# Kernel tuning notes

Measured on AMD Instinct MI355X. Metric: run time of the kernel, lower is better.

The kernel has to match this reference:

```python
import jax, jax.numpy as jnp
import numpy as np
from jax import lax

NUM_LAYERS = 128
SEQ_LEN = 256
H = 1  # hidden_size = input_size = 1


def setup_inputs() -> dict:
    key = jax.random.key(0)
    k = jax.random.split(key, 5)
    # PyTorch GRU init: U(-1/sqrt(H), 1/sqrt(H)) with H=1 -> U(-1, 1)
    u = lambda kk, shp: jax.random.uniform(kk, shp, jnp.float32, -1.0, 1.0)
    return {
        "x": jax.random.normal(k[0], (1, SEQ_LEN), jnp.float32),
        "w_ih": u(k[1], (NUM_LAYERS, 3 * H, H)),  # gates stacked [r, z, n]
        "w_hh": u(k[2], (NUM_LAYERS, 3 * H, H)),
        "b_ih": u(k[3], (NUM_LAYERS, 3 * H)),
        "b_hh": u(k[4], (NUM_LAYERS, 3 * H)),
    }


def _gru_stack(x_seq, w_ih, w_hh, b_ih, b_hh):
    # x_seq: [T, H]; params stacked over layers. PyTorch GRU equations, gate order r,z,n.
    def layer_step(seq, params):
        wi, wh, bi, bh = params  # [3H,H], [3H,H], [3H], [3H]

        def cell(h, xt):  # h: [H], xt: [H]
            gi = wi @ xt + bi  # [3H]
            gh = wh @ h + bh   # [3H]
            r = jax.nn.sigmoid(gi[0:H] + gh[0:H])
            z = jax.nn.sigmoid(gi[H:2 * H] + gh[H:2 * H])
            n = jnp.tanh(gi[2 * H:] + r * gh[2 * H:])
            h_new = (1.0 - z) * n + z * h
            return h_new, h_new

        h0 = jnp.zeros((H,), dtype=seq.dtype)
        _, out = lax.scan(cell, h0, seq)  # out: [T, H]
        return out, None

    out, _ = lax.scan(layer_step, x_seq, (w_ih, w_hh, b_ih, b_hh))
    return out


def reference(x, w_ih, w_hh, b_ih, b_hh):
    # x: [1, T] -> GRU input [T, H=1] (unbatched), encoder only (decoder unused in forward)
    seq = x.T  # [T, 1]
    out = _gru_stack(seq, w_ih, w_hh, b_ih, b_hh)  # [T, 1]
    return out.T  # [1, T]
```

## Files before the change

kernel.cpp:

```cpp
#include <hip/hip_runtime.h>

#define T_LEN 256
#define NG 26

__device__ __forceinline__ float ex2(float x) { return __builtin_amdgcn_exp2f(x); }
__device__ __forceinline__ float rcp1p(float e) { return __builtin_amdgcn_rcpf(1.0f + e); }

__device__ __forceinline__ float dpp_wave_shr1(float v) {
    int i = __float_as_int(v);
    return __int_as_float(__builtin_amdgcn_update_dpp(i, i, 0x138, 0xF, 0xF, false));
}
__device__ __forceinline__ float dpp_wave_rol1(float v) {
    int i = __float_as_int(v);
    return __int_as_float(__builtin_amdgcn_update_dpp(i, i, 0x134, 0xF, 0xF, false));
}

__global__ __launch_bounds__(128, 1) void gru_stack_wavefront(
    const float* __restrict__ x,
    const float* __restrict__ w_ih,
    const float* __restrict__ w_hh,
    const float* __restrict__ b_ih,
    const float* __restrict__ b_hh,
    float* __restrict__ out)
{
    __shared__ float ring[2 * 64 * 64];
    const int tid  = threadIdx.x;
    const int lane = tid & 63;
    const int wid  = tid >> 6;

    #pragma unroll 4
    for (int m = tid; m < 2 * 64 * 64; m += 128) ring[m] = 0.0f;

    const float L1 = -1.4426950408889634f;
    const float L2 = -2.8853900817779268f;

    const float wi_r = L1 * w_ih[3 * tid + 0], wh_r = L1 * w_hh[3 * tid + 0];
    const float b_r  = L1 * (b_ih[3 * tid + 0] + b_hh[3 * tid + 0]);
    const float wi_z = L1 * w_ih[3 * tid + 1], wh_z = L1 * w_hh[3 * tid + 1];
    const float b_z  = L1 * (b_ih[3 * tid + 1] + b_hh[3 * tid + 1]);
    const float wi_n = L2 * w_ih[3 * tid + 2], bi_n = L2 * b_ih[3 * tid + 2];
    const float wh_n = L2 * w_hh[3 * tid + 2], bh_n = L2 * b_hh[3 * tid + 2];

    float xc0 = x[lane];
    float xc1 = x[lane + 64];
    float xc2 = x[lane + 128];
    float xc3 = x[lane + 192];

    float h = 0.0f;
    float c_r = b_r, c_z = b_z, g_n = bh_n;

    float pcur[16], pnext[16];
    #pragma unroll
    for (int k = 0; k < 16; ++k) { pcur[k] = 0.0f; pnext[k] = 0.0f; }

    float ov = 0.0f;
    float xq = xc0;
    int t = -lane - 96 * wid - 1;

    const bool is_l0 = (lane == 0);
    const bool is_w1 = (wid == 1);
    float* ringw = &ring[wid * 4096];

    __syncthreads();

    for (int g = 0; g < NG; ++g) {
        if      (g == 4)  xq = xc1;
        else if (g == 8)  xq = xc2;
        else if (g == 12) xq = xc3;

        if (is_w1) {
            const int base = 16 * g - 17;
            #pragma unroll
            for (int k = 0; k < 16; ++k)
                pnext[k] = ring[((base + k) & 63) * 64 + 63];
        }

        const int sb = (16 * g) & 63;

        #pragma unroll
        for (int k = 0; k < 16; ++k) {
            ++t;
            const bool valid = (unsigned)t < (unsigned)T_LEN;

            float alt = is_w1 ? pcur[k] : xq;
            float shifted = dpp_wave_shr1(h);
            float in = is_l0 ? alt : shifted;

            float u_r  = fmaf(wi_r, in, c_r);
            float u_z  = fmaf(wi_z, in, c_z);
            float u_n0 = fmaf(wi_n, in, bi_n);
            float r = rcp1p(ex2(u_r));
            float z = rcp1p(ex2(u_z));
            z = valid ? z : 1.0f;
            float n = fmaf(2.0f, rcp1p(ex2(fmaf(r, g_n, u_n0))), -1.0f);
            h = fmaf(z, h - n, n);

            c_r = fmaf(wh_r, h, b_r);
            c_z = fmaf(wh_z, h, b_z);
            g_n = fmaf(wh_n, h, bh_n);

            ringw[((sb + k) & 63) * 64 + lane] = h;

            float rot = dpp_wave_rol1(ov);
            ov = (lane == 63) ? h : rot;
            xq = dpp_wave_rol1(xq);

            if (k == 14) {
                if (is_w1 && (g & 3) == 1 && g >= 13)
                    out[16 * g - 208 + lane] = ov;
            }
        }

        if (is_w1) {
            #pragma unroll
            for (int k = 0; k < 16; ++k) pcur[k] = pnext[k];
        }
        __syncthreads();
    }
}

extern "C" void kernel_launch(void* const* d_in, const int* in_sizes, int n_in,
                              void* d_out, int out_size, void* d_ws, size_t ws_size,
                              hipStream_t stream) {
    const float* x    = (const float*)d_in[0];
    const float* w_ih = (const float*)d_in[1];
    const float* w_hh = (const float*)d_in[2];
    const float* b_ih = (const float*)d_in[3];
    const float* b_hh = (const float*)d_in[4];
    float* out = (float*)d_out;

    gru_stack_wavefront<<<1, 128, 0, stream>>>(x, w_ih, w_hh, b_ih, b_hh, out);
}
```

Measured before the change: 95.78 us.

## Split r/z gates across lane pairs and run four waves of 32 layers

Each layer now occupies two lanes, one computing the r gate and one the z gate, so the dependent chain per step has one sigmoid and a pair-swap instead of two sigmoids. The 128 layers are spread over four wavefronts of 32 layers, with 16-step blocks passed between waves through shared-memory rings and barrier-synchronised. Input x is staged in LDS, and the output is written directly by the last thread instead of through a rotating output register. This shortens per-step latency but doubles the shift per step and adds one more group of steps and a deeper inter-wave pipeline.

```diff
diff --git a/kernel.cpp b/kernel.cpp
--- a/kernel.cpp
+++ b/kernel.cpp
@@ -1,7 +1,7 @@
 #include <hip/hip_runtime.h>
 
 #define T_LEN 256
-#define NG 26
+#define NG 27
 
 __device__ __forceinline__ float ex2(float x) { return __builtin_amdgcn_exp2f(x); }
 __device__ __forceinline__ float rcp1p(float e) { return __builtin_amdgcn_rcpf(1.0f + e); }
@@ -10,12 +10,12 @@
     int i = __float_as_int(v);
     return __int_as_float(__builtin_amdgcn_update_dpp(i, i, 0x138, 0xF, 0xF, false));
 }
-__device__ __forceinline__ float dpp_wave_rol1(float v) {
+__device__ __forceinline__ float dpp_pair_swap(float v) {
     int i = __float_as_int(v);
-    return __int_as_float(__builtin_amdgcn_update_dpp(i, i, 0x134, 0xF, 0xF, false));
+    return __int_as_float(__builtin_amdgcn_update_dpp(i, i, 0xB1, 0xF, 0xF, false));
 }
 
-__global__ __launch_bounds__(128, 1) void gru_stack_wavefront(
+__global__ __launch_bounds__(256, 1) void gru_stack_wavefront(
     const float* __restrict__ x,
     const float* __restrict__ w_ih,
     const float* __restrict__ w_hh,
@@ -23,97 +23,79 @@
     const float* __restrict__ b_hh,
     float* __restrict__ out)
 {
-    __shared__ float ring[2 * 64 * 64];
+    __shared__ float ring[4 * 64 * 64];
+    __shared__ float sx[T_LEN];
     const int tid  = threadIdx.x;
     const int lane = tid & 63;
     const int wid  = tid >> 6;
+    const int j    = lane >> 1;
+    const int p    = lane & 1;
+    const int L    = 32 * wid + j;
 
-    #pragma unroll 4
-    for (int m = tid; m < 2 * 64 * 64; m += 128) ring[m] = 0.0f;
+    sx[tid & (T_LEN - 1)] = x[tid & (T_LEN - 1)];
+    #pragma unroll
+    for (int m = tid; m < 4 * 64 * 64; m += 256) ring[m] = 0.0f;
 
     const float L1 = -1.4426950408889634f;
     const float L2 = -2.8853900817779268f;
 
-    const float wi_r = L1 * w_ih[3 * tid + 0], wh_r = L1 * w_hh[3 * tid + 0];
-    const float b_r  = L1 * (b_ih[3 * tid + 0] + b_hh[3 * tid + 0]);
-    const float wi_z = L1 * w_ih[3 * tid + 1], wh_z = L1 * w_hh[3 * tid + 1];
-    const float b_z  = L1 * (b_ih[3 * tid + 1] + b_hh[3 * tid + 1]);
-    const float wi_n = L2 * w_ih[3 * tid + 2], bi_n = L2 * b_ih[3 * tid + 2];
-    const float wh_n = L2 * w_hh[3 * tid + 2], bh_n = L2 * b_hh[3 * tid + 2];
-
-    float xc0 = x[lane];
-    float xc1 = x[lane + 64];
-    float xc2 = x[lane + 128];
-    float xc3 = x[lane + 192];
+    const float wi_rz = L1 * w_ih[3 * L + p], wh_rz = L1 * w_hh[3 * L + p];
+    const float b_rz  = L1 * (b_ih[3 * L + p] + b_hh[3 * L + p]);
+    const float wi_n = L2 * w_ih[3 * L + 2], bi_n = L2 * b_ih[3 * L + 2];
+    const float wh_n = L2 * w_hh[3 * L + 2], bh_n = L2 * b_hh[3 * L + 2];
 
     float h = 0.0f;
-    float c_r = b_r, c_z = b_z, g_n = bh_n;
+    float c_rz = b_rz, g_n = bh_n;
 
-    float pcur[16], pnext[16];
-    #pragma unroll
-    for (int k = 0; k < 16; ++k) { pcur[k] = 0.0f; pnext[k] = 0.0f; }
-
-    float ov = 0.0f;
-    float xq = xc0;
-    int t = -lane - 96 * wid - 1;
-
-    const bool is_l0 = (lane == 0);
-    const bool is_w1 = (wid == 1);
-    float* ringw = &ring[wid * 4096];
+    const int  toff   = j + 48 * wid;
+    const bool seam   = (lane < 2);
+    const bool w0     = (wid == 0);
+    const bool isout  = (tid == 255);
+    float pk[16];
 
     __syncthreads();
 
     for (int g = 0; g < NG; ++g) {
-        if      (g == 4)  xq = xc1;
-        else if (g == 8)  xq = xc2;
-        else if (g == 12) xq = xc3;
+        const int sb = 16 * g;
 
-        if (is_w1) {
-            const int base = 16 * g - 17;
+        if (w0) {
             #pragma unroll
             for (int k = 0; k < 16; ++k)
-                pnext[k] = ring[((base + k) & 63) * 64 + 63];
+                pk[k] = sx[(sb + k) & (T_LEN - 1)];
+        } else {
+            const float* plane = &ring[(wid - 1) * 4096];
+            #pragma unroll
+            for (int k = 0; k < 16; ++k)
+                pk[k] = plane[((sb + k - 17) & 63) * 64 + 62];
         }
-
-        const int sb = (16 * g) & 63;
 
         #pragma unroll
         for (int k = 0; k < 16; ++k) {
-            ++t;
-            const bool valid = (unsigned)t < (unsigned)T_LEN;
+            const int s = sb + k;
+            const bool valid = (unsigned)(s - toff) < (unsigned)T_LEN;
 
-            float alt = is_w1 ? pcur[k] : xq;
-            float shifted = dpp_wave_shr1(h);
-            float in = is_l0 ? alt : shifted;
+            float s1 = dpp_wave_shr1(h);
+            float s2 = dpp_wave_shr1(s1);
+            float in = seam ? pk[k] : s2;
 
-            float u_r  = fmaf(wi_r, in, c_r);
-            float u_z  = fmaf(wi_z, in, c_z);
-            float u_n0 = fmaf(wi_n, in, bi_n);
-            float r = rcp1p(ex2(u_r));
-            float z = rcp1p(ex2(u_z));
-            z = valid ? z : 1.0f;
-            float n = fmaf(2.0f, rcp1p(ex2(fmaf(r, g_n, u_n0))), -1.0f);
-            h = fmaf(z, h - n, n);
+            float u   = fmaf(wi_rz, in, c_rz);
+            float un0 = fmaf(wi_n,  in, bi_n);
+            float rz  = rcp1p(ex2(u));
+            float other = dpp_pair_swap(rz);
+            float rv = p ? other : rz;
+            float zv = p ? rz : other;
+            zv = valid ? zv : 1.0f;
 
-            c_r = fmaf(wh_r, h, b_r);
-            c_z = fmaf(wh_z, h, b_z);
-            g_n = fmaf(wh_n, h, bh_n);
+            float un = fmaf(rv, g_n, un0);
+            float n  = fmaf(2.0f, rcp1p(ex2(un)), -1.0f);
+            h = fmaf(zv, h - n, n);
 
-            ringw[((sb + k) & 63) * 64 + lane] = h;
+            c_rz = fmaf(wh_rz, h, b_rz);
+            g_n  = fmaf(wh_n,  h, bh_n);
 
-            float rot = dpp_wave_rol1(ov);
-            ov = (lane == 63) ? h : rot;
-            xq = dpp_wave_rol1(xq);
+            ring[wid * 4096 + (s & 63) * 64 + lane] = h;
 
-            if (k == 14) {
-                if (is_w1 && (g & 3) == 1 && g >= 13)
-                    out[16 * g - 208 + lane] = ov;
-            }
-        }
-
-        if (is_w1) {
-            #pragma unroll
-            for (int k = 0; k < 16; ++k) pcur[k] = pnext[k];
+            if (isout && valid) out[s - 175] = h;
         }
         __syncthreads();
     }
@@ -129,5 +111,5 @@
     const float* b_hh = (const float*)d_in[4];
     float* out = (float*)d_out;
 
-    gru_stack_wavefront<<<1, 128, 0, stream>>>(x, w_ih, w_hh, b_ih, b_hh, out);
+    gru_stack_wavefront<<<1, 256, 0, stream>>>(x, w_ih, w_hh, b_ih, b_hh, out);
 }
```

Result: slower. 105.5 us (+10.1%).

## Restructure GRU wavefront inputs: stage x in LDS, hoist DPP shift, shorten the gate chain

Applied to the files above, without the earlier changes.

The input for the next step (DPP shift of h, or the lane-0 boundary value) is now computed at the end of each step, so it is ready before the next iteration begins. x is staged in shared memory and read per group, replacing the rotating register queue. Only wave 0 writes its last-layer plane to the ring, and wave 1 reads the boundary values straight from that plane. The output is written directly by thread 127 every step instead of being collected through a rotating DPP register. The hidden-state update is rearranged algebraically so more of it runs in parallel with the tanh exp/rcp chain. The risk is extra scattered global stores from a single lane and a changed read latency between the two waves.

```diff
diff --git a/kernel.cpp b/kernel.cpp
--- a/kernel.cpp
+++ b/kernel.cpp
@@ -4,15 +4,11 @@
 #define NG 26
 
 __device__ __forceinline__ float ex2(float x) { return __builtin_amdgcn_exp2f(x); }
-__device__ __forceinline__ float rcp1p(float e) { return __builtin_amdgcn_rcpf(1.0f + e); }
+__device__ __forceinline__ float rcpf_(float x) { return __builtin_amdgcn_rcpf(x); }
 
 __device__ __forceinline__ float dpp_wave_shr1(float v) {
     int i = __float_as_int(v);
     return __int_as_float(__builtin_amdgcn_update_dpp(i, i, 0x138, 0xF, 0xF, false));
-}
-__device__ __forceinline__ float dpp_wave_rol1(float v) {
-    int i = __float_as_int(v);
-    return __int_as_float(__builtin_amdgcn_update_dpp(i, i, 0x134, 0xF, 0xF, false));
 }
 
 __global__ __launch_bounds__(128, 1) void gru_stack_wavefront(
@@ -23,13 +19,16 @@
     const float* __restrict__ b_hh,
     float* __restrict__ out)
 {
-    __shared__ float ring[2 * 64 * 64];
+    __shared__ float plane0[64 * 64];
+    __shared__ float sx[T_LEN];
     const int tid  = threadIdx.x;
     const int lane = tid & 63;
     const int wid  = tid >> 6;
 
-    #pragma unroll 4
-    for (int m = tid; m < 2 * 64 * 64; m += 128) ring[m] = 0.0f;
+    sx[tid] = x[tid];
+    sx[tid + 128] = x[tid + 128];
+    #pragma unroll
+    for (int m = tid; m < 64 * 64; m += 128) plane0[m] = 0.0f;
 
     const float L1 = -1.4426950408889634f;
     const float L2 = -2.8853900817779268f;
@@ -41,79 +40,58 @@
     const float wi_n = L2 * w_ih[3 * tid + 2], bi_n = L2 * b_ih[3 * tid + 2];
     const float wh_n = L2 * w_hh[3 * tid + 2], bh_n = L2 * b_hh[3 * tid + 2];
 
-    float xc0 = x[lane];
-    float xc1 = x[lane + 64];
-    float xc2 = x[lane + 128];
-    float xc3 = x[lane + 192];
+    const float x0 = x[0];
 
     float h = 0.0f;
     float c_r = b_r, c_z = b_z, g_n = bh_n;
 
-    float pcur[16], pnext[16];
-    #pragma unroll
-    for (int k = 0; k < 16; ++k) { pcur[k] = 0.0f; pnext[k] = 0.0f; }
+    const bool is_l0 = (lane == 0);
+    const bool is_w0 = (wid == 0);
 
-    float ov = 0.0f;
-    float xq = xc0;
+    float in = (is_l0 && is_w0) ? x0 : 0.0f;
+
+    float pk[16];
     int t = -lane - 96 * wid - 1;
-
-    const bool is_l0 = (lane == 0);
-    const bool is_w1 = (wid == 1);
-    float* ringw = &ring[wid * 4096];
 
     __syncthreads();
 
     for (int g = 0; g < NG; ++g) {
-        if      (g == 4)  xq = xc1;
-        else if (g == 8)  xq = xc2;
-        else if (g == 12) xq = xc3;
-
-        if (is_w1) {
-            const int base = 16 * g - 17;
+        if (is_w0) {
             #pragma unroll
             for (int k = 0; k < 16; ++k)
-                pnext[k] = ring[((base + k) & 63) * 64 + 63];
+                pk[k] = sx[(16 * g + k + 1) & (T_LEN - 1)];
+        } else {
+            #pragma unroll
+            for (int k = 0; k < 16; ++k)
+                pk[k] = plane0[((16 * g + k - 32) & 63) * 64 + 63];
         }
-
-        const int sb = (16 * g) & 63;
 
         #pragma unroll
         for (int k = 0; k < 16; ++k) {
             ++t;
             const bool valid = (unsigned)t < (unsigned)T_LEN;
 
-            float alt = is_w1 ? pcur[k] : xq;
-            float shifted = dpp_wave_shr1(h);
-            float in = is_l0 ? alt : shifted;
-
-            float u_r  = fmaf(wi_r, in, c_r);
-            float u_z  = fmaf(wi_z, in, c_z);
-            float u_n0 = fmaf(wi_n, in, bi_n);
-            float r = rcp1p(ex2(u_r));
-            float z = rcp1p(ex2(u_z));
+            float u_r = fmaf(wi_r, in, c_r);
+            float u_z = fmaf(wi_z, in, c_z);
+            float bse = fmaf(wi_n, in, bi_n);
+            float r = rcpf_(1.0f + ex2(u_r));
+            float z = rcpf_(1.0f + ex2(u_z));
             z = valid ? z : 1.0f;
-            float n = fmaf(2.0f, rcp1p(ex2(fmaf(r, g_n, u_n0))), -1.0f);
-            h = fmaf(z, h - n, n);
+            float two_omz = fmaf(-2.0f, z, 2.0f);
+            float zh_m = fmaf(z, h, z - 1.0f);
+            float un = fmaf(r, g_n, bse);
+            float s_n = rcpf_(1.0f + ex2(un));
+            h = fmaf(s_n, two_omz, zh_m);
 
             c_r = fmaf(wh_r, h, b_r);
             c_z = fmaf(wh_z, h, b_z);
             g_n = fmaf(wh_n, h, bh_n);
 
-            ringw[((sb + k) & 63) * 64 + lane] = h;
+            if (is_w0) plane0[((16 * g + k) & 63) * 64 + lane] = h;
+            if (tid == 127 && valid) out[t] = h;
 
-            float rot = dpp_wave_rol1(ov);
-            ov = (lane == 63) ? h : rot;
-            xq = dpp_wave_rol1(xq);
-
-            if (k == 14) {
-                if (is_w1 && (g & 3) == 1 && g >= 13)
-                    out[16 * g - 208 + lane] = ov;
-            }
-        }
-
-        if (is_w1) {
-            #pragma unroll
-            for (int k = 0; k < 16; ++k) pcur[k] = pnext[k];
+            float sh = dpp_wave_shr1(h);
+            in = is_l0 ? pk[k] : sh;
         }
         __syncthreads();
     }
```

Result: no change. 97.66 us (+2.0%).

## Shrink GRU wavefront groups to 8 steps and tighten inter-wave lag

Applied to the files above, without the earlier changes.

Cuts the per-barrier group from 16 to 8 timesteps and lowers the wave-1 lag from 96 to 73 steps, so the total pipeline is 49×8 steps instead of 26×16. This shortens the diagonal fill and drain at the cost of twice as many block barriers. The change also stores only wave 0's outputs to a single LDS plane and drops the register double-buffer for wave 1's inputs. It adds a steady-state branch that skips the validity masking on z.

```diff
diff --git a/kernel.cpp b/kernel.cpp
--- a/kernel.cpp
+++ b/kernel.cpp
@@ -1,7 +1,7 @@
 #include <hip/hip_runtime.h>
 
 #define T_LEN 256
-#define NG 26
+#define NGROUP 49
 
 __device__ __forceinline__ float ex2(float x) { return __builtin_amdgcn_exp2f(x); }
 __device__ __forceinline__ float rcp1p(float e) { return __builtin_amdgcn_rcpf(1.0f + e); }
@@ -23,13 +23,13 @@
     const float* __restrict__ b_hh,
     float* __restrict__ out)
 {
-    __shared__ float ring[2 * 64 * 64];
+    __shared__ float plane0[64 * 64];
     const int tid  = threadIdx.x;
     const int lane = tid & 63;
     const int wid  = tid >> 6;
 
-    #pragma unroll 4
-    for (int m = tid; m < 2 * 64 * 64; m += 128) ring[m] = 0.0f;
+    #pragma unroll
+    for (int m = tid; m < 64 * 64; m += 128) plane0[m] = 0.0f;
 
     const float L1 = -1.4426950408889634f;
     const float L2 = -2.8853900817779268f;
@@ -49,71 +49,88 @@
     float h = 0.0f;
     float c_r = b_r, c_z = b_z, g_n = bh_n;
 
-    float pcur[16], pnext[16];
-    #pragma unroll
-    for (int k = 0; k < 16; ++k) { pcur[k] = 0.0f; pnext[k] = 0.0f; }
-
+    float pk[8];
     float ov = 0.0f;
     float xq = xc0;
-    int t = -lane - 96 * wid - 1;
 
     const bool is_l0 = (lane == 0);
-    const bool is_w1 = (wid == 1);
-    float* ringw = &ring[wid * 4096];
+    const bool is_w0 = (wid == 0);
+    const bool is_w1 = !is_w0;
 
     __syncthreads();
 
-    for (int g = 0; g < NG; ++g) {
-        if      (g == 4)  xq = xc1;
-        else if (g == 8)  xq = xc2;
-        else if (g == 12) xq = xc3;
-
-        if (is_w1) {
-            const int base = 16 * g - 17;
-            #pragma unroll
-            for (int k = 0; k < 16; ++k)
-                pnext[k] = ring[((base + k) & 63) * 64 + 63];
-        }
-
-        const int sb = (16 * g) & 63;
-
-        #pragma unroll
-        for (int k = 0; k < 16; ++k) {
-            ++t;
-            const bool valid = (unsigned)t < (unsigned)T_LEN;
-
-            float alt = is_w1 ? pcur[k] : xq;
-            float shifted = dpp_wave_shr1(h);
-            float in = is_l0 ? alt : shifted;
-
-            float u_r  = fmaf(wi_r, in, c_r);
-            float u_z  = fmaf(wi_z, in, c_z);
-            float u_n0 = fmaf(wi_n, in, bi_n);
-            float r = rcp1p(ex2(u_r));
-            float z = rcp1p(ex2(u_z));
-            z = valid ? z : 1.0f;
-            float n = fmaf(2.0f, rcp1p(ex2(fmaf(r, g_n, u_n0))), -1.0f);
-            h = fmaf(z, h - n, n);
-
-            c_r = fmaf(wh_r, h, b_r);
-            c_z = fmaf(wh_z, h, b_z);
-            g_n = fmaf(wh_n, h, bh_n);
-
-            ringw[((sb + k) & 63) * 64 + lane] = h;
-
-            float rot = dpp_wave_rol1(ov);
-            ov = (lane == 63) ? h : rot;
-            xq = dpp_wave_rol1(xq);
-
-            if (k == 14) {
-                if (is_w1 && (g & 3) == 1 && g >= 13)
-                    out[16 * g - 208 + lane] = ov;
-            }
-        }
+    for (int g = 0; g < NGROUP; ++g) {
+        if      (g == 8)  xq = xc1;
+        else if (g == 16) xq = xc2;
+        else if (g == 24) xq = xc3;
 
         if (is_w1) {
             #pragma unroll
-            for (int k = 0; k < 16; ++k) pcur[k] = pnext[k];
+            for (int k = 0; k < 8; ++k)
+                pk[k] = plane0[((8 * g + k - 10) & 63) * 64 + 63];
+        }
+
+        const int tb = 8 * g - lane - 73 * wid;
+        const bool steady = is_w0 ? (g >= 8 && g <= 31) : (g >= 17 && g <= 40);
+
+        if (steady) {
+            #pragma unroll
+            for (int k = 0; k < 8; ++k) {
+                float alt = is_w1 ? pk[k] : xq;
+                float shifted = dpp_wave_shr1(h);
+                float in = is_l0 ? alt : shifted;
+
+                float u_r = fmaf(wi_r, in, c_r);
+                float u_z = fmaf(wi_z, in, c_z);
+                float bse = fmaf(wi_n, in, bi_n);
+                float r = rcp1p(ex2(u_r));
+                float z = rcp1p(ex2(u_z));
+                float n = fmaf(2.0f, rcp1p(ex2(fmaf(r, g_n, bse))), -1.0f);
+                h = fmaf(z, h - n, n);
+
+                c_r = fmaf(wh_r, h, b_r);
+                c_z = fmaf(wh_z, h, b_z);
+                g_n = fmaf(wh_n, h, bh_n);
+
+                if (is_w0) plane0[((8 * g + k) & 63) * 64 + lane] = h;
+
+                float rot = dpp_wave_rol1(ov);
+                ov = (lane == 63) ? h : rot;
+                xq = dpp_wave_rol1(xq);
+
+                if (k == 7 && is_w1 && g >= 24 && ((g - 24) & 7) == 0)
+                    out[8 * g - 192 + lane] = ov;
+            }
+        } else {
+            #pragma unroll
+            for (int k = 0; k < 8; ++k) {
+                float alt = is_w1 ? pk[k] : xq;
+                float shifted = dpp_wave_shr1(h);
+                float in = is_l0 ? alt : shifted;
+
+                float u_r = fmaf(wi_r, in, c_r);
+                float u_z = fmaf(wi_z, in, c_z);
+                float bse = fmaf(wi_n, in, bi_n);
+                float r = rcp1p(ex2(u_r));
+                float z = rcp1p(ex2(u_z));
+                const bool valid = (unsigned)(tb + k) < (unsigned)T_LEN;
+                z = valid ? z : 1.0f;
+                float n = fmaf(2.0f, rcp1p(ex2(fmaf(r, g_n, bse))), -1.0f);
+                h = fmaf(z, h - n, n);
+
+                c_r = fmaf(wh_r, h, b_r);
+                c_z = fmaf(wh_z, h, b_z);
+                g_n = fmaf(wh_n, h, bh_n);
+
+                if (is_w0) plane0[((8 * g + k) & 63) * 64 + lane] = h;
+
+                float rot = dpp_wave_rol1(ov);
+                ov = (lane == 63) ? h : rot;
+                xq = dpp_wave_rol1(xq);
+
+                if (k == 7 && is_w1 && g >= 24 && ((g - 24) & 7) == 0)
+                    out[8 * g - 192 + lane] = ov;
+            }
         }
         __syncthreads();
     }
```

New measurement: 98.99 us. 1.03x slower.
